# Optimization experiments

Measured on AMD Instinct MI355X. Metric: run time of the kernel, lower is better.

## Reference

```python
import jax, jax.numpy as jnp
from jax import lax
import numpy as np

B = 16384
D = 32
N_HEADS = 4


def _piece_table():
    base = np.zeros((7, 4, 4), np.int32)
    cells = [
        [(1, 0), (1, 1), (1, 2), (1, 3)],  # I
        [(1, 1), (1, 2), (2, 1), (2, 2)],  # O
        [(1, 1), (2, 0), (2, 1), (2, 2)],  # T
        [(1, 1), (1, 2), (2, 0), (2, 1)],  # S
        [(1, 0), (1, 1), (2, 1), (2, 2)],  # Z
        [(1, 0), (2, 0), (2, 1), (2, 2)],  # J
        [(1, 2), (2, 0), (2, 1), (2, 2)],  # L
    ]
    for i, cs in enumerate(cells):
        for (r, c) in cs:
            base[i, r, c] = 1
    rots = np.stack([np.stack([np.rot90(base[i], k) for k in range(4)]) for i in range(7)])
    p = np.concatenate([rots, np.zeros((1, 4, 4, 4), np.int32)], 0)  # [8,4,4,4]
    return jnp.asarray(p)


def setup_inputs() -> dict:
    key = jax.random.key(0)
    ks = jax.random.split(key, 24)

    def ri(k, n, lo, hi):
        return jax.random.randint(k, (B, n), lo, hi, dtype=jnp.int32)

    t = jnp.concatenate([
        ri(ks[0], 1, 0, 10),   # col0 feature
        ri(ks[1], 1, 2, 8),
        ri(ks[2], 1, 0, 10),   # col2 y pos
        ri(ks[3], 1, 0, 8),    # col3 drop dist
        ri(ks[4], 1, 0, 4),    # col4 rotation
        ri(ks[5], 3, 0, 10),   # cols5-7
        ri(ks[6], 1, 0, 7),    # col8 piece id
        ri(ks[7], 6, 0, 7),    # cols9-14 hold/next
        ri(ks[8], 7, 0, 10),   # cols15-21
        ri(ks[9], 210, 0, 2),  # cols22-231 board
    ], axis=1)

    s = 0.05
    rn = lambda k, shp: jax.random.normal(k, shp, jnp.float32) * s
    return {
        "t": t,
        "piece_table": _piece_table(),
        "conv1_w": rn(ks[10], (6, 3, 5, 5)), "conv1_b": rn(ks[11], (6,)),
        "conv2_w": rn(ks[12], (16, 6, 5, 5)), "conv2_b": rn(ks[13], (16,)),
        "conv3_w": rn(ks[14], (64, 16, 3, 1)), "conv3_b": rn(ks[15], (64,)),
        "lfc1_w": rn(ks[16], (32, 64)), "lfc1_b": rn(ks[17], (32,)),
        "fc_w": rn(ks[18], (32, 8)), "fc_b": rn(ks[19], (32,)),
        "emb": rn(ks[20], (8, D)),
        "in_proj_w": rn(ks[21], (3 * D, D)), "in_proj_b": jnp.zeros((3 * D,), jnp.float32),
        "out_proj_w": rn(ks[22], (D, D)), "out_proj_b": jnp.zeros((D,), jnp.float32),
    }


def _avgpool2(x):
    b, c, h, w = x.shape
    h2, w2 = h // 2, w // 2
    return x[:, :, :h2 * 2, :w2 * 2].reshape(b, c, h2, 2, w2, 2).mean((3, 5))


def _lenet(x, w1, b1, w2, b2, w3, b3, fw, fb):
    dn = ("NCHW", "OIHW", "NCHW")
    x = jax.nn.relu(lax.conv_general_dilated(x, w1, (1, 1), ((2, 2), (2, 2)), dimension_numbers=dn) + b1[None, :, None, None])
    x = _avgpool2(x)                                   # [B,6,11,6]
    x = jax.nn.relu(lax.conv_general_dilated(x, w2, (1, 1), ((0, 0), (0, 0)), dimension_numbers=dn) + b2[None, :, None, None])
    x = _avgpool2(x)                                   # [B,16,3,1]
    x = jax.nn.relu(lax.conv_general_dilated(x, w3, (1, 1), ((0, 0), (0, 0)), dimension_numbers=dn) + b3[None, :, None, None])
    x = x.reshape(-1, 64)
    return jax.nn.relu(x @ fw.T + fb)                  # [B,32]


def _pe():
    pos = jnp.array([0, 0, 1, 2, 3, 4, 5], jnp.float32)[:, None]
    div = jnp.exp(jnp.arange(0, D, 2, dtype=jnp.float32) * (-jnp.log(10000.0) / D))
    s, c = jnp.sin(pos * div), jnp.cos(pos * div)      # [7,16] each
    return jnp.stack([s, c], -1).reshape(7, D)         # interleaved sin/cos


def _mha(q_in, kv, in_w, in_b, out_w, out_b):
    qw, kw, vw = in_w[:D], in_w[D:2 * D], in_w[2 * D:]
    qb, kb, vb = in_b[:D], in_b[D:2 * D], in_b[2 * D:]
    b, lq, _ = q_in.shape
    hd = D // N_HEADS
    q = (q_in @ qw.T + qb).reshape(b, lq, N_HEADS, hd)
    k = (kv @ kw.T + kb).reshape(b, -1, N_HEADS, hd)
    v = (kv @ vw.T + vb).reshape(b, -1, N_HEADS, hd)
    scores = jnp.einsum("bqhd,bkhd->bhqk", q, k) / jnp.sqrt(jnp.float32(hd))
    w = jax.nn.softmax(scores, axis=-1)
    o = jnp.einsum("bhqk,bkhd->bqhd", w, v).reshape(b, lq, D)
    return o @ out_w.T + out_b


def reference(t, piece_table, conv1_w, conv1_b, conv2_w, conv2_b, conv3_w, conv3_b,
              lfc1_w, lfc1_b, fc_w, fc_b, emb, in_proj_w, in_proj_b, out_proj_w, out_proj_b):
    bsz = t.shape[0]
    board = jnp.zeros((bsz, 3, 21, 10), jnp.float32)
    board = board.at[:, 0].set(t[:, 22:232].astype(jnp.float32).reshape(bsz, 21, 10))

    # gather piece grid, extract the 4 filled cells per sample in row-major order
    pieces = piece_table[t[:, 8], t[:, 4]].reshape(bsz, 16)        # [B,16] in {0,1}
    idx = jnp.argsort(1 - pieces, axis=1, stable=True)[:, :4]      # first 4 ones, scan order
    cy, cx = idx // 4, idx % 4
    x = cx + t[:, 1][:, None] - 2
    y = cy + t[:, 2][:, None]
    ny = y + t[:, 3][:, None]
    mask = (y >= 0) & (ny >= 0)
    br = jnp.arange(bsz, dtype=jnp.int32)[:, None]
    y_m = jnp.where(mask, y, -1)
    ny_m = jnp.where(mask, ny, -1)
    board = board.at[br, 1, y_m, x].set(1.0, mode="drop")
    board = board.at[br, 2, ny_m, x].set(1.0, mode="drop")

    board = jnp.pad(board, ((0, 0), (0, 0), (0, 1), (1, 1)), constant_values=1.0)  # [B,3,22,12]

    t9 = jnp.where((t[:, 9] != -1) & (t[:, 6] != 0), t[:, 9], 7)
    hold_next = jnp.concatenate([t[:, 8:9], t9[:, None], t[:, 10:15]], axis=1)     # [B,7]

    b2 = _lenet(board, conv1_w, conv1_b, conv2_w, conv2_b, conv3_w, conv3_b, lfc1_w, lfc1_b)  # [B,32]
    bkv = b2[:, None, :]                                            # [B,1,32]
    p = emb[hold_next] + _pe()[None]                                # [B,7,32]
    a = _mha(p, bkv, in_proj_w, in_proj_b, out_proj_w, out_proj_b)  # [B,7,32]

    xf = jax.nn.relu(t[:, :8].astype(jnp.float32) @ fc_w.T + fc_b)  # [B,32]
    out = jnp.concatenate([xf, a.mean(axis=1), b2], axis=1)         # [B,96]
    return (out, board)
```

## Files before the change

kernel.cpp:

```cpp
#include <hip/hip_runtime.h>
#include <cstddef>


typedef float f32x2 __attribute__((ext_vector_type(2)));

#define BATCH 16384
#define SPB   4
#define NBLK  (BATCH / SPB)
#define RS    18
#define P1OFF  432
#define PCSOFF 800
#define SS2    816

__global__ __launch_bounds__(256)
void cborder_kernel(const float* __restrict__ w1, float* __restrict__ cb)
{
  int i = blockIdx.x * 256 + threadIdx.x;
  if (i >= 1584) return;
  int p = i / 6, o = i - p * 6;
  int y0 = p / 12, x0 = p - y0 * 12;
  float acc = 0.f;
#pragma unroll
  for (int dy = 0; dy < 5; ++dy)
#pragma unroll
    for (int dx = 0; dx < 5; ++dx) {
      int pr = y0 + dy - 2, pc = x0 + dx - 2;
      if (pr >= 0 && pr < 22 && pc >= 0 && pc < 12 &&
          (pr == 21 || pc == 0 || pc == 11)) {
        int k = dy * 5 + dx;
        acc += w1[(o * 3 + 0) * 25 + k] + w1[(o * 3 + 1) * 25 + k]
             + w1[(o * 3 + 2) * 25 + k];
      }
    }
  cb[i] = acc;
}

__global__ __launch_bounds__(256)
void board_model_kernel(const int* __restrict__ t,
                        const int* __restrict__ piece_table,
                        const float* __restrict__ w1, const float* __restrict__ b1,
                        const float* __restrict__ w2, const float* __restrict__ b2w,
                        const float* __restrict__ w3, const float* __restrict__ b3,
                        const float* __restrict__ wf1, const float* __restrict__ bf1,
                        const float* __restrict__ fcw, const float* __restrict__ fcb,
                        const float* __restrict__ ipw, const float* __restrict__ ipb,
                        const float* __restrict__ opw, const float* __restrict__ opb,
                        const float* __restrict__ cbg,
                        float* __restrict__ out,
                        float* __restrict__ out_board)
{
  __shared__ __align__(16) float scr[SPB * SS2];
  __shared__ float cbL[1440];

  const int tid  = threadIdx.x;
  const int lane = tid & 63;
  const int wv   = tid >> 6;
  const int s    = blockIdx.x * SPB + wv;

  float* W   = &scr[wv * SS2];
  int*   pcs = (int*)&scr[wv * SS2 + PCSOFF];
  const int* tr = t + (size_t)s * 232;

  for (int i = lane; i < 1440; i += 64) cbL[i] = cbg[i];

  {
    float4* W4 = (float4*)W;
    for (int i = lane; i < 108; i += 64) W4[i] = float4{0.f, 0.f, 0.f, 0.f};

    for (int i = lane; i < 210; i += 64) {
      int r = i / 10, b = i - r * 10;
      W[(r + 2) * RS + b + 5] = (float)tr[22 + i];
    }

    if (lane < 4) {
      const int* pt = piece_table + (tr[8] * 4 + tr[4]) * 16;
      int sel = -1, n1 = 0;
#pragma unroll
      for (int j = 0; j < 16; ++j) { if (pt[j]) { if (n1 == lane) sel = j; ++n1; } }
      if (sel < 0) {
        int n0 = 0, want = lane - n1;
#pragma unroll
        for (int j = 0; j < 16; ++j) if (!pt[j]) { if (n0 == want) { sel = j; break; } ++n0; }
      }
      int cy = sel >> 2, cx = sel & 3;
      int x  = cx + tr[1] - 2;
      int y  = cy + tr[2];
      int ny = y + tr[3];
      bool mask = (y >= 0) && (ny >= 0);
      bool xok  = (x >= 0) && (x < 10);
      bool v1 = mask && xok && (y < 21);
      bool v2 = mask && xok && (ny < 21);
      pcs[2 * lane + 0]       = v1 ? y  : -100;
      pcs[2 * lane + 1]       = x + 1;
      pcs[2 * (lane + 4)]     = v2 ? ny : -100;
      pcs[2 * (lane + 4) + 1] = x + 1;
    }
  }
  __threadfence_block();
  __builtin_amdgcn_wave_barrier();

  {
    float* ob = out_board + (size_t)s * 792;
    for (int v = lane; v < 198; v += 64) {
      int j0 = v * 4;
      int ch = j0 / 264, rem = j0 - ch * 264;
      int r = rem / 12, c = rem - r * 12;
      float val[4];
      if (ch == 0) {
#pragma unroll
        for (int d = 0; d < 4; ++d) {
          int cd = c + d;
          val[d] = (r == 21 || cd == 0 || cd == 11) ? 1.f
                 : W[(r + 2) * RS + cd + 4];
        }
      } else {
#pragma unroll
        for (int d = 0; d < 4; ++d) {
          int cd = c + d;
          val[d] = (r == 21 || cd == 0 || cd == 11) ? 1.f : 0.f;
        }
#pragma unroll
        for (int e = 0; e < 4; ++e) {
          int pr = pcs[2 * ((ch - 1) * 4 + e)];
          int pc = pcs[2 * ((ch - 1) * 4 + e) + 1];
          if (pr == r && (unsigned)(pc - c) < 4u) val[pc - c] = 1.f;
        }
      }
      *(float4*)(ob + j0) = float4{val[0], val[1], val[2], val[3]};
    }
  }

  if (lane < 60) {
    int p = lane;
    int r = p / 6, c = p - r * 6;
    float acc[2][2][6];
#pragma unroll
    for (int i = 0; i < 2; ++i)
#pragma unroll
      for (int j = 0; j < 2; ++j) {
        int pcell = (2 * r + i) * 12 + (2 * c + j);
#pragma unroll
        for (int o = 0; o < 6; ++o)
          acc[i][j][o] = b1[o] + cbL[pcell * 6 + o];
      }

    {
      const float* base = W + (2 * r) * RS + (2 * c + 2);
#pragma unroll
      for (int u = 0; u < 6; ++u) {
        float2 a0 = *(const float2*)(base + u * RS);
        float2 a1 = *(const float2*)(base + u * RS + 2);
        float2 a2 = *(const float2*)(base + u * RS + 4);
        float rv[6] = {a0.x, a0.y, a1.x, a1.y, a2.x, a2.y};
#pragma unroll
        for (int i = 0; i < 2; ++i) {
          if (u - i < 0 || u - i > 4) continue;
          const int ky = u - i;
#pragma unroll
          for (int j = 0; j < 2; ++j)
#pragma unroll
            for (int kx = 0; kx < 5; ++kx) {
              float xv = rv[j + kx];
#pragma unroll
              for (int o = 0; o < 6; ++o)
                acc[i][j][o] += xv * w1[o * 75 + ky * 5 + kx];
            }
        }
      }
    }

#pragma unroll
    for (int e = 0; e < 8; ++e) {
      int pr = pcs[2 * e];
      if (pr < 0) continue;
      int pc = pcs[2 * e + 1];
      int chm = e >> 2;
      int dyb = pr + 2 - 2 * r;
      int dxb = pc + 2 - 2 * c;
      if (dyb < 0 || dyb > 5 || dxb < 0 || dxb > 5) continue;
#pragma unroll
      for (int i = 0; i < 2; ++i) {
        int dy = dyb - i;
        if ((unsigned)dy >= 5u) continue;
#pragma unroll
        for (int j = 0; j < 2; ++j) {
          int dx = dxb - j;
          if ((unsigned)dx >= 5u) continue;
#pragma unroll
          for (int o = 0; o < 6; ++o)
            acc[i][j][o] += w1[(o * 3 + 1 + chm) * 25 + dy * 5 + dx];
        }
      }
    }

    float* P1q = W + P1OFF;
#pragma unroll
    for (int o = 0; o < 6; ++o) {
      float v = fmaxf(acc[0][0][o], 0.f) + fmaxf(acc[0][1][o], 0.f)
              + fmaxf(acc[1][0][o], 0.f) + fmaxf(acc[1][1][o], 0.f);
      P1q[o * 61 + p] = 0.25f * v;
    }
  }
  __threadfence_block();
  __builtin_amdgcn_wave_barrier();

  {
    const int oc = lane >> 2;
    const int pq = lane & 3;
    const int r0 = pq >> 1, c0 = pq & 1;
    const float* P1q = W + P1OFF;
    float a3[3];
    float bv = b2w[oc];
    a3[0] = bv; a3[1] = bv; a3[2] = bv;
    for (int ic = 0; ic < 6; ++ic) {
      float wch[25];
#pragma unroll
      for (int j = 0; j < 25; ++j)
        wch[j] = w2[oc * 150 + ic * 25 + j];
#pragma unroll
      for (int u = 0; u < 9; ++u) {
        float xv[5];
#pragma unroll
        for (int kc = 0; kc < 5; ++kc)
          xv[kc] = P1q[ic * 61 + (r0 + u) * 6 + c0 + kc];
        if (u <= 4) {
#pragma unroll
          for (int kc = 0; kc < 5; ++kc) a3[0] += xv[kc] * wch[u * 5 + kc];
        }
        if (u >= 2 && u <= 6) {
#pragma unroll
          for (int kc = 0; kc < 5; ++kc) a3[1] += xv[kc] * wch[(u - 2) * 5 + kc];
        }
        if (u >= 4) {
#pragma unroll
          for (int kc = 0; kc < 5; ++kc) a3[2] += xv[kc] * wch[(u - 4) * 5 + kc];
        }
      }
    }
    W[oc * 12 + pq]     = fmaxf(a3[0], 0.f);
    W[oc * 12 + pq + 4] = fmaxf(a3[1], 0.f);
    W[oc * 12 + pq + 8] = fmaxf(a3[2], 0.f);
  }
  __threadfence_block();
  __builtin_amdgcn_wave_barrier();

  {
    float* S = W;

    if (lane < 48) {
      int o = lane / 3, pr = lane - o * 3;
      float v = 0.25f * (S[o * 12 + 4 * pr] + S[o * 12 + 4 * pr + 1]
                       + S[o * 12 + 4 * pr + 2] + S[o * 12 + 4 * pr + 3]);
      S[192 + lane] = v;
    }
    __threadfence_block();
    __builtin_amdgcn_wave_barrier();

    {
      int o = lane;
      const f32x2* w3r = (const f32x2*)(w3 + o * 48);
      f32x2 accp = f32x2{b3[o], 0.f};
#pragma unroll
      for (int k2 = 0; k2 < 24; ++k2)
        accp += *(const f32x2*)(S + 192 + 2 * k2) * w3r[k2];
      S[240 + o] = fmaxf(accp.x + accp.y, 0.f);
    }
    __threadfence_block();
    __builtin_amdgcn_wave_barrier();

    {
      int j = lane & 31, h = lane >> 5;
      const f32x2* wr = (const f32x2*)(wf1 + j * 64 + 32 * h);
      f32x2 accp = f32x2{0.f, 0.f};
#pragma unroll
      for (int k2 = 0; k2 < 16; ++k2)
        accp += *(const f32x2*)(S + 240 + 32 * h + 2 * k2) * wr[k2];
      float part = accp.x + accp.y;
      part += __shfl_xor(part, 32, 64);
      if (h == 0) {
        float acc = fmaxf(bf1[j] + part, 0.f);
        S[304 + j] = acc;
        out[(size_t)s * 96 + 64 + j] = acc;
      }
    }
    __threadfence_block();
    __builtin_amdgcn_wave_barrier();

    {
      int j = lane & 31;
      if (lane < 32) {
        const f32x2* wr = (const f32x2*)(ipw + (64 + j) * 32);
        f32x2 accp = f32x2{ipb[64 + j], 0.f};
#pragma unroll
        for (int k2 = 0; k2 < 16; ++k2)
          accp += *(const f32x2*)(S + 304 + 2 * k2) * wr[k2];
        S[336 + j] = accp.x + accp.y;
      } else {
        const f32x2* wr = (const f32x2*)(fcw + j * 8);
        f32x2 accp = f32x2{fcb[j], 0.f};
#pragma unroll
        for (int k2 = 0; k2 < 4; ++k2) {
          f32x2 tv = f32x2{(float)tr[2 * k2], (float)tr[2 * k2 + 1]};
          accp += tv * wr[k2];
        }
        out[(size_t)s * 96 + j] = fmaxf(accp.x + accp.y, 0.f);
      }
    }
    __threadfence_block();
    __builtin_amdgcn_wave_barrier();

    if (lane < 32) {
      int j = lane;
      const f32x2* wr = (const f32x2*)(opw + j * 32);
      f32x2 accp = f32x2{opb[j], 0.f};
#pragma unroll
      for (int k2 = 0; k2 < 16; ++k2)
        accp += *(const f32x2*)(S + 336 + 2 * k2) * wr[k2];
      out[(size_t)s * 96 + 32 + j] = accp.x + accp.y;
    }
  }
}

extern "C" void kernel_launch(void* const* d_in, const int* in_sizes, int n_in,
                              void* d_out, int out_size, void* d_ws, size_t ws_size,
                              hipStream_t stream) {
  const int*   t   = (const int*)d_in[0];
  const int*   pt  = (const int*)d_in[1];
  const float* w1  = (const float*)d_in[2];
  const float* b1  = (const float*)d_in[3];
  const float* w2  = (const float*)d_in[4];
  const float* b2w = (const float*)d_in[5];
  const float* w3  = (const float*)d_in[6];
  const float* b3  = (const float*)d_in[7];
  const float* wf1 = (const float*)d_in[8];
  const float* bf1 = (const float*)d_in[9];
  const float* fcw = (const float*)d_in[10];
  const float* fcb = (const float*)d_in[11];
  const float* ipw = (const float*)d_in[13];
  const float* ipb = (const float*)d_in[14];
  const float* opw = (const float*)d_in[15];
  const float* opb = (const float*)d_in[16];

  float* out       = (float*)d_out;
  float* out_board = out + (size_t)BATCH * 96;
  float* cbg       = (float*)d_ws;

  hipLaunchKernelGGL(cborder_kernel, dim3(7), dim3(256), 0, stream, w1, cbg);
  hipLaunchKernelGGL(board_model_kernel, dim3(NBLK), dim3(256), 0, stream,
                     t, pt, w1, b1, w2, b2w, w3, b3, wf1, bf1, fcw, fcb,
                     ipw, ipb, opw, opb, cbg, out, out_board);
}
```

Baseline: 219.5 us.

## Map one sample per half-wave and use packed FP32 math in convolutions

Each 32-lane half-wave now handles one sample, so a block of 256 threads covers 8 samples instead of 4. Conv1 computes two pooled outputs per lane using pre-transposed weights packed as f32x2, which a precompute kernel writes to workspace. Conv2 computes row pairs with packed multiplies and does its 2x2 pooling through a lane shuffle. The later FC stages are reshaped to run on 32 lanes. The aim is to raise lane utilisation and issue fewer scalar FMAs, at the cost of higher register pressure and longer per-lane serial work in the FC stages.

```diff
diff --git a/kernel.cpp b/kernel.cpp
--- a/kernel.cpp
+++ b/kernel.cpp
@@ -5,34 +5,39 @@
 typedef float f32x2 __attribute__((ext_vector_type(2)));
 
 #define BATCH 16384
-#define SPB   4
+#define SPB   8
 #define NBLK  (BATCH / SPB)
 #define RS    18
-#define P1OFF  432
-#define PCSOFF 800
-#define SS2    816
+#define SS2    464
+#define P1S    62
+#define WS_W1P 1584
 
 __global__ __launch_bounds__(256)
-void cborder_kernel(const float* __restrict__ w1, float* __restrict__ cb)
+void precomp_kernel(const float* __restrict__ w1, float* __restrict__ ws)
 {
   int i = blockIdx.x * 256 + threadIdx.x;
-  if (i >= 1584) return;
-  int p = i / 6, o = i - p * 6;
-  int y0 = p / 12, x0 = p - y0 * 12;
-  float acc = 0.f;
-#pragma unroll
-  for (int dy = 0; dy < 5; ++dy)
-#pragma unroll
-    for (int dx = 0; dx < 5; ++dx) {
-      int pr = y0 + dy - 2, pc = x0 + dx - 2;
-      if (pr >= 0 && pr < 22 && pc >= 0 && pc < 12 &&
-          (pr == 21 || pc == 0 || pc == 11)) {
-        int k = dy * 5 + dx;
-        acc += w1[(o * 3 + 0) * 25 + k] + w1[(o * 3 + 1) * 25 + k]
-             + w1[(o * 3 + 2) * 25 + k];
-      }
-    }
-  cb[i] = acc;
+  if (i < 1584) {
+    int p = i / 6, o = i - p * 6;
+    int y0 = p / 12, x0 = p - y0 * 12;
+    float acc = 0.f;
+#pragma unroll
+    for (int dy = 0; dy < 5; ++dy)
+#pragma unroll
+      for (int dx = 0; dx < 5; ++dx) {
+        int pr = y0 + dy - 2, pc = x0 + dx - 2;
+        if (pr >= 0 && pr < 22 && pc >= 0 && pc < 12 &&
+            (pr == 21 || pc == 0 || pc == 11)) {
+          int k = dy * 5 + dx;
+          acc += w1[(o * 3 + 0) * 25 + k] + w1[(o * 3 + 1) * 25 + k]
+               + w1[(o * 3 + 2) * 25 + k];
+        }
+      }
+    ws[i] = acc;
+  } else if (i < 1734) {
+    int j = i - 1584;
+    int tap = j / 6, o = j - tap * 6;
+    ws[i] = w1[o * 75 + tap];
+  }
 }
 
 __global__ __launch_bounds__(256)
@@ -45,40 +50,42 @@
                         const float* __restrict__ fcw, const float* __restrict__ fcb,
                         const float* __restrict__ ipw, const float* __restrict__ ipb,
                         const float* __restrict__ opw, const float* __restrict__ opb,
-                        const float* __restrict__ cbg,
+                        const float* __restrict__ ws,
                         float* __restrict__ out,
                         float* __restrict__ out_board)
 {
   __shared__ __align__(16) float scr[SPB * SS2];
   __shared__ float cbL[1440];
 
-  const int tid  = threadIdx.x;
-  const int lane = tid & 63;
-  const int wv   = tid >> 6;
-  const int s    = blockIdx.x * SPB + wv;
-
-  float* W   = &scr[wv * SS2];
-  int*   pcs = (int*)&scr[wv * SS2 + PCSOFF];
+  const int tid = threadIdx.x;
+  const int l   = tid & 31;
+  const int u   = tid >> 5;
+  const int s   = blockIdx.x * SPB + u;
+
+  const f32x2* w1p2 = (const f32x2*)(ws + WS_W1P);
+
+  float* W   = &scr[u * SS2];
+  int*   pcs = (int*)&scr[u * SS2 + 448];
   const int* tr = t + (size_t)s * 232;
 
-  for (int i = lane; i < 1440; i += 64) cbL[i] = cbg[i];
+  for (int i = tid; i < 1440; i += 256) cbL[i] = ws[i];
 
   {
     float4* W4 = (float4*)W;
-    for (int i = lane; i < 108; i += 64) W4[i] = float4{0.f, 0.f, 0.f, 0.f};
-
-    for (int i = lane; i < 210; i += 64) {
+    for (int i = l; i < 108; i += 32) W4[i] = float4{0.f, 0.f, 0.f, 0.f};
+
+    for (int i = l; i < 210; i += 32) {
       int r = i / 10, b = i - r * 10;
       W[(r + 2) * RS + b + 5] = (float)tr[22 + i];
     }
 
-    if (lane < 4) {
+    if (l < 4) {
       const int* pt = piece_table + (tr[8] * 4 + tr[4]) * 16;
       int sel = -1, n1 = 0;
 #pragma unroll
-      for (int j = 0; j < 16; ++j) { if (pt[j]) { if (n1 == lane) sel = j; ++n1; } }
+      for (int j = 0; j < 16; ++j) { if (pt[j]) { if (n1 == l) sel = j; ++n1; } }
       if (sel < 0) {
-        int n0 = 0, want = lane - n1;
+        int n0 = 0, want = l - n1;
 #pragma unroll
         for (int j = 0; j < 16; ++j) if (!pt[j]) { if (n0 == want) { sel = j; break; } ++n0; }
       }
@@ -90,18 +97,17 @@
       bool xok  = (x >= 0) && (x < 10);
       bool v1 = mask && xok && (y < 21);
       bool v2 = mask && xok && (ny < 21);
-      pcs[2 * lane + 0]       = v1 ? y  : -100;
-      pcs[2 * lane + 1]       = x + 1;
-      pcs[2 * (lane + 4)]     = v2 ? ny : -100;
-      pcs[2 * (lane + 4) + 1] = x + 1;
-    }
-  }
-  __threadfence_block();
-  __builtin_amdgcn_wave_barrier();
+      pcs[2 * l + 0]       = v1 ? y  : -100;
+      pcs[2 * l + 1]       = x + 1;
+      pcs[2 * (l + 4)]     = v2 ? ny : -100;
+      pcs[2 * (l + 4) + 1] = x + 1;
+    }
+  }
+  __syncthreads();
 
   {
     float* ob = out_board + (size_t)s * 792;
-    for (int v = lane; v < 198; v += 64) {
+    for (int v = l; v < 198; v += 32) {
       int j0 = v * 4;
       int ch = j0 / 264, rem = j0 - ch * 264;
       int r = rem / 12, c = rem - r * 12;
@@ -130,193 +136,221 @@
     }
   }
 
-  if (lane < 60) {
-    int p = lane;
-    int r = p / 6, c = p - r * 6;
-    float acc[2][2][6];
-#pragma unroll
-    for (int i = 0; i < 2; ++i)
-#pragma unroll
-      for (int j = 0; j < 2; ++j) {
-        int pcell = (2 * r + i) * 12 + (2 * c + j);
-#pragma unroll
-        for (int o = 0; o < 6; ++o)
-          acc[i][j][o] = b1[o] + cbL[pcell * 6 + o];
-      }
-
-    {
-      const float* base = W + (2 * r) * RS + (2 * c + 2);
-#pragma unroll
-      for (int u = 0; u < 6; ++u) {
-        float2 a0 = *(const float2*)(base + u * RS);
-        float2 a1 = *(const float2*)(base + u * RS + 2);
-        float2 a2 = *(const float2*)(base + u * RS + 4);
-        float rv[6] = {a0.x, a0.y, a1.x, a1.y, a2.x, a2.y};
+  float p1v[2][6];
+  {
+    const int r  = (2 * l) / 6;
+    const int ca = 2 * l - r * 6;
+    f32x2 acc2[2][2][2][3];
+    if (l < 30) {
+#pragma unroll
+      for (int pos = 0; pos < 2; ++pos)
+#pragma unroll
+        for (int i = 0; i < 2; ++i)
+#pragma unroll
+          for (int j = 0; j < 2; ++j) {
+            int pcell = (2 * r + i) * 12 + (2 * (ca + pos) + j);
+#pragma unroll
+            for (int o2 = 0; o2 < 3; ++o2) {
+              f32x2 cb2 = *(const f32x2*)&cbL[pcell * 6 + 2 * o2];
+              acc2[pos][i][j][o2] = f32x2{b1[2 * o2] + cb2.x, b1[2 * o2 + 1] + cb2.y};
+            }
+          }
+
+      const float* base = W + (2 * r) * RS + (2 * ca + 2);
+#pragma unroll
+      for (int uu = 0; uu < 6; ++uu) {
+        float2 a0 = *(const float2*)(base + uu * RS);
+        float2 a1 = *(const float2*)(base + uu * RS + 2);
+        float2 a2 = *(const float2*)(base + uu * RS + 4);
+        float2 a3 = *(const float2*)(base + uu * RS + 6);
+        float rv[8] = {a0.x, a0.y, a1.x, a1.y, a2.x, a2.y, a3.x, a3.y};
 #pragma unroll
         for (int i = 0; i < 2; ++i) {
-          if (u - i < 0 || u - i > 4) continue;
-          const int ky = u - i;
-#pragma unroll
-          for (int j = 0; j < 2; ++j)
-#pragma unroll
-            for (int kx = 0; kx < 5; ++kx) {
-              float xv = rv[j + kx];
+          if (uu - i < 0 || uu - i > 4) continue;
+          const int ky = uu - i;
+#pragma unroll
+          for (int kx = 0; kx < 5; ++kx) {
+            const int tap = ky * 5 + kx;
+#pragma unroll
+            for (int pos = 0; pos < 2; ++pos)
+#pragma unroll
+              for (int j = 0; j < 2; ++j) {
+                float xv = rv[2 * pos + j + kx];
+#pragma unroll
+                for (int o2 = 0; o2 < 3; ++o2)
+                  acc2[pos][i][j][o2] += w1p2[tap * 3 + o2] * f32x2{xv, xv};
+              }
+          }
+        }
+      }
+
+#pragma unroll
+      for (int e = 0; e < 8; ++e) {
+        int pr = pcs[2 * e];
+        if (pr < 0) continue;
+        int pc = pcs[2 * e + 1];
+        int chm = e >> 2;
+#pragma unroll
+        for (int pos = 0; pos < 2; ++pos) {
+          int dyb = pr + 2 - 2 * r;
+          int dxb = pc + 2 - 2 * (ca + pos);
+          if (dyb < 0 || dyb > 5 || dxb < 0 || dxb > 5) continue;
+#pragma unroll
+          for (int i = 0; i < 2; ++i) {
+            int dy = dyb - i;
+            if ((unsigned)dy >= 5u) continue;
+#pragma unroll
+            for (int j = 0; j < 2; ++j) {
+              int dx = dxb - j;
+              if ((unsigned)dx >= 5u) continue;
 #pragma unroll
               for (int o = 0; o < 6; ++o)
-                acc[i][j][o] += xv * w1[o * 75 + ky * 5 + kx];
+                acc2[pos][i][j][o >> 1][o & 1] += w1[(o * 3 + 1 + chm) * 25 + dy * 5 + dx];
             }
-        }
-      }
-    }
-
-#pragma unroll
-    for (int e = 0; e < 8; ++e) {
-      int pr = pcs[2 * e];
-      if (pr < 0) continue;
-      int pc = pcs[2 * e + 1];
-      int chm = e >> 2;
-      int dyb = pr + 2 - 2 * r;
-      int dxb = pc + 2 - 2 * c;
-      if (dyb < 0 || dyb > 5 || dxb < 0 || dxb > 5) continue;
-#pragma unroll
-      for (int i = 0; i < 2; ++i) {
-        int dy = dyb - i;
-        if ((unsigned)dy >= 5u) continue;
-#pragma unroll
-        for (int j = 0; j < 2; ++j) {
-          int dx = dxb - j;
-          if ((unsigned)dx >= 5u) continue;
-#pragma unroll
-          for (int o = 0; o < 6; ++o)
-            acc[i][j][o] += w1[(o * 3 + 1 + chm) * 25 + dy * 5 + dx];
-        }
-      }
-    }
-
-    float* P1q = W + P1OFF;
-#pragma unroll
-    for (int o = 0; o < 6; ++o) {
-      float v = fmaxf(acc[0][0][o], 0.f) + fmaxf(acc[0][1][o], 0.f)
-              + fmaxf(acc[1][0][o], 0.f) + fmaxf(acc[1][1][o], 0.f);
-      P1q[o * 61 + p] = 0.25f * v;
+          }
+        }
+      }
+
+#pragma unroll
+      for (int pos = 0; pos < 2; ++pos)
+#pragma unroll
+        for (int o = 0; o < 6; ++o) {
+          int o2 = o >> 1, ob = o & 1;
+          p1v[pos][o] = 0.25f * (fmaxf(acc2[pos][0][0][o2][ob], 0.f)
+                               + fmaxf(acc2[pos][0][1][o2][ob], 0.f)
+                               + fmaxf(acc2[pos][1][0][o2][ob], 0.f)
+                               + fmaxf(acc2[pos][1][1][o2][ob], 0.f));
+        }
     }
   }
   __threadfence_block();
   __builtin_amdgcn_wave_barrier();
 
-  {
-    const int oc = lane >> 2;
-    const int pq = lane & 3;
-    const int r0 = pq >> 1, c0 = pq & 1;
-    const float* P1q = W + P1OFF;
-    float a3[3];
+  if (l < 30) {
+#pragma unroll
+    for (int o = 0; o < 6; ++o)
+      *(f32x2*)&W[o * P1S + 2 * l] = f32x2{p1v[0][o], p1v[1][o]};
+  }
+  __threadfence_block();
+  __builtin_amdgcn_wave_barrier();
+
+  float p2a = 0.f, p2b = 0.f;
+  {
+    const int oc = l >> 1;
+    const int rb = l & 1;
+    f32x2 a[3];
     float bv = b2w[oc];
-    a3[0] = bv; a3[1] = bv; a3[2] = bv;
+    a[0] = f32x2{bv, bv}; a[1] = f32x2{bv, bv}; a[2] = f32x2{bv, bv};
     for (int ic = 0; ic < 6; ++ic) {
       float wch[25];
 #pragma unroll
       for (int j = 0; j < 25; ++j)
         wch[j] = w2[oc * 150 + ic * 25 + j];
-#pragma unroll
-      for (int u = 0; u < 9; ++u) {
-        float xv[5];
-#pragma unroll
-        for (int kc = 0; kc < 5; ++kc)
-          xv[kc] = P1q[ic * 61 + (r0 + u) * 6 + c0 + kc];
-        if (u <= 4) {
-#pragma unroll
-          for (int kc = 0; kc < 5; ++kc) a3[0] += xv[kc] * wch[u * 5 + kc];
-        }
-        if (u >= 2 && u <= 6) {
-#pragma unroll
-          for (int kc = 0; kc < 5; ++kc) a3[1] += xv[kc] * wch[(u - 2) * 5 + kc];
-        }
-        if (u >= 4) {
-#pragma unroll
-          for (int kc = 0; kc < 5; ++kc) a3[2] += xv[kc] * wch[(u - 4) * 5 + kc];
-        }
-      }
-    }
-    W[oc * 12 + pq]     = fmaxf(a3[0], 0.f);
-    W[oc * 12 + pq + 4] = fmaxf(a3[1], 0.f);
-    W[oc * 12 + pq + 8] = fmaxf(a3[2], 0.f);
+      const float* P1r = W + ic * P1S + (3 * rb) * 6;
+#pragma unroll
+      for (int uu = 0; uu < 7; ++uu) {
+        float2 b0 = *(const float2*)(P1r + uu * 6);
+        float2 b1v = *(const float2*)(P1r + uu * 6 + 2);
+        float2 b2v = *(const float2*)(P1r + uu * 6 + 4);
+        float rv[6] = {b0.x, b0.y, b1v.x, b1v.y, b2v.x, b2v.y};
+#pragma unroll
+        for (int ri = 0; ri < 3; ++ri) {
+          int ky = uu - ri;
+          if (ky < 0 || ky > 4) continue;
+#pragma unroll
+          for (int kc = 0; kc < 5; ++kc)
+            a[ri] += f32x2{rv[kc], rv[kc + 1]} * f32x2{wch[ky * 5 + kc], wch[ky * 5 + kc]};
+        }
+      }
+    }
+    float rs[3];
+#pragma unroll
+    for (int ri = 0; ri < 3; ++ri)
+      rs[ri] = fmaxf(a[ri].x, 0.f) + fmaxf(a[ri].y, 0.f);
+    float partner = rs[rb == 0 ? 2 : 0];
+    float other = __shfl_xor(partner, 1, 64);
+    p2a = (rb == 0) ? 0.25f * (rs[0] + rs[1]) : 0.25f * (rs[0] + other);
+    p2b = (rb == 0) ? 0.f                     : 0.25f * (rs[1] + rs[2]);
+    if (rb == 0) p2b = 0.25f * (rs[2] + other);
   }
   __threadfence_block();
   __builtin_amdgcn_wave_barrier();
 
   {
+    const int oc = l >> 1;
+    const int rb = l & 1;
+    if (rb == 0) {
+      W[oc * 3 + 0] = p2a;
+      W[oc * 3 + 1] = p2b;
+    } else {
+      W[oc * 3 + 2] = p2b;
+    }
+  }
+  __threadfence_block();
+  __builtin_amdgcn_wave_barrier();
+
+  {
     float* S = W;
 
-    if (lane < 48) {
-      int o = lane / 3, pr = lane - o * 3;
-      float v = 0.25f * (S[o * 12 + 4 * pr] + S[o * 12 + 4 * pr + 1]
-                       + S[o * 12 + 4 * pr + 2] + S[o * 12 + 4 * pr + 3]);
-      S[192 + lane] = v;
+#pragma unroll
+    for (int half = 0; half < 2; ++half) {
+      int o = l + 32 * half;
+      const f32x2* w3r = (const f32x2*)(w3 + o * 48);
+      f32x2 accp = f32x2{b3[o], 0.f};
+#pragma unroll
+      for (int k2 = 0; k2 < 24; ++k2)
+        accp += *(const f32x2*)(S + 2 * k2) * w3r[k2];
+      S[64 + o] = fmaxf(accp.x + accp.y, 0.f);
     }
     __threadfence_block();
     __builtin_amdgcn_wave_barrier();
 
     {
-      int o = lane;
-      const f32x2* w3r = (const f32x2*)(w3 + o * 48);
-      f32x2 accp = f32x2{b3[o], 0.f};
-#pragma unroll
-      for (int k2 = 0; k2 < 24; ++k2)
-        accp += *(const f32x2*)(S + 192 + 2 * k2) * w3r[k2];
-      S[240 + o] = fmaxf(accp.x + accp.y, 0.f);
+      int j = l;
+      const f32x2* wr = (const f32x2*)(wf1 + j * 64);
+      f32x2 accp = f32x2{bf1[j], 0.f};
+#pragma unroll
+      for (int k2 = 0; k2 < 32; ++k2)
+        accp += *(const f32x2*)(S + 64 + 2 * k2) * wr[k2];
+      float acc = fmaxf(accp.x + accp.y, 0.f);
+      S[144 + j] = acc;
+      out[(size_t)s * 96 + 64 + j] = acc;
     }
     __threadfence_block();
     __builtin_amdgcn_wave_barrier();
 
     {
-      int j = lane & 31, h = lane >> 5;
-      const f32x2* wr = (const f32x2*)(wf1 + j * 64 + 32 * h);
-      f32x2 accp = f32x2{0.f, 0.f};
+      int j = l;
+      const f32x2* wr = (const f32x2*)(ipw + (64 + j) * 32);
+      f32x2 accp = f32x2{ipb[64 + j], 0.f};
 #pragma unroll
       for (int k2 = 0; k2 < 16; ++k2)
-        accp += *(const f32x2*)(S + 240 + 32 * h + 2 * k2) * wr[k2];
-      float part = accp.x + accp.y;
-      part += __shfl_xor(part, 32, 64);
-      if (h == 0) {
-        float acc = fmaxf(bf1[j] + part, 0.f);
-        S[304 + j] = acc;
-        out[(size_t)s * 96 + 64 + j] = acc;
-      }
+        accp += *(const f32x2*)(S + 144 + 2 * k2) * wr[k2];
+      S[176 + j] = accp.x + accp.y;
     }
     __threadfence_block();
     __builtin_amdgcn_wave_barrier();
 
     {
-      int j = lane & 31;
-      if (lane < 32) {
-        const f32x2* wr = (const f32x2*)(ipw + (64 + j) * 32);
-        f32x2 accp = f32x2{ipb[64 + j], 0.f};
-#pragma unroll
-        for (int k2 = 0; k2 < 16; ++k2)
-          accp += *(const f32x2*)(S + 304 + 2 * k2) * wr[k2];
-        S[336 + j] = accp.x + accp.y;
-      } else {
-        const f32x2* wr = (const f32x2*)(fcw + j * 8);
-        f32x2 accp = f32x2{fcb[j], 0.f};
-#pragma unroll
-        for (int k2 = 0; k2 < 4; ++k2) {
-          f32x2 tv = f32x2{(float)tr[2 * k2], (float)tr[2 * k2 + 1]};
-          accp += tv * wr[k2];
-        }
-        out[(size_t)s * 96 + j] = fmaxf(accp.x + accp.y, 0.f);
-      }
-    }
-    __threadfence_block();
-    __builtin_amdgcn_wave_barrier();
-
-    if (lane < 32) {
-      int j = lane;
+      int j = l;
       const f32x2* wr = (const f32x2*)(opw + j * 32);
       f32x2 accp = f32x2{opb[j], 0.f};
 #pragma unroll
       for (int k2 = 0; k2 < 16; ++k2)
-        accp += *(const f32x2*)(S + 336 + 2 * k2) * wr[k2];
+        accp += *(const f32x2*)(S + 176 + 2 * k2) * wr[k2];
       out[(size_t)s * 96 + 32 + j] = accp.x + accp.y;
+    }
+
+    {
+      int j = l;
+      const f32x2* wr = (const f32x2*)(fcw + j * 8);
+      f32x2 accp = f32x2{fcb[j], 0.f};
+#pragma unroll
+      for (int k2 = 0; k2 < 4; ++k2) {
+        f32x2 tv = f32x2{(float)tr[2 * k2], (float)tr[2 * k2 + 1]};
+        accp += tv * wr[k2];
+      }
+      out[(size_t)s * 96 + j] = fmaxf(accp.x + accp.y, 0.f);
     }
   }
 }
@@ -343,10 +377,10 @@
 
   float* out       = (float*)d_out;
   float* out_board = out + (size_t)BATCH * 96;
-  float* cbg       = (float*)d_ws;
-
-  hipLaunchKernelGGL(cborder_kernel, dim3(7), dim3(256), 0, stream, w1, cbg);
+  float* ws        = (float*)d_ws;
+
+  hipLaunchKernelGGL(precomp_kernel, dim3(7), dim3(256), 0, stream, w1, ws);
   hipLaunchKernelGGL(board_model_kernel, dim3(NBLK), dim3(256), 0, stream,
                      t, pt, w1, b1, w2, b2w, w3, b3, wf1, bf1, fcw, fcb,
-                     ipw, ipb, opw, opb, cbg, out, out_board);
+                     ipw, ipb, opw, opb, ws, out, out_board);
 }
```

Result: faster. 214.7 us (-2.2%).
